# Kernel optimization log

Hardware: AMD Instinct MI355X
Metric: run time of the kernel (lower is better)

## Reference

```python
import jax, jax.numpy as jnp
import numpy as np

NEG_SLOPE = 0.2  # PyG GATConv default negative_slope


def _gat_layer(x, src, dst, W, a_src, a_dst, b, heads, ch, concat, num_nodes):
    # x: [Nt, Fin]; W: [Fin, heads*ch]; a_src/a_dst: [heads, ch]
    xw = (x @ W).reshape(num_nodes, heads, ch)            # [Nt, H, C]
    alpha_s = jnp.sum(xw * a_src, axis=-1)                # [Nt, H]
    alpha_d = jnp.sum(xw * a_dst, axis=-1)                # [Nt, H]
    e = jax.nn.leaky_relu(alpha_s[src] + alpha_d[dst], NEG_SLOPE)  # [E, H]
    # segment softmax over destination nodes (every node has a self-loop)
    m = jax.lax.stop_gradient(jax.ops.segment_max(e, dst, num_segments=num_nodes))
    ex = jnp.exp(e - m[dst])
    denom = jax.ops.segment_sum(ex, dst, num_segments=num_nodes)
    alpha = ex / (denom[dst] + 1e-16)                     # [E, H]
    out = jax.ops.segment_sum(alpha[:, :, None] * xw[src], dst, num_segments=num_nodes)  # [Nt, H, C]
    out = out.reshape(num_nodes, heads * ch) if concat else out.mean(axis=1)
    return out + b


def setup_inputs() -> dict:
    key = jax.random.key(0)
    ks = jax.random.split(key, 12)
    B, N, IN, HID, H, OUT, E = 2, 10000, 256, 256, 2, 256, 160000
    x = jax.random.normal(ks[0], (B, N, IN), dtype=jnp.float32)
    edge_index = jax.random.randint(ks[1], (2, E), 0, N, dtype=jnp.int32)
    s_in = 1.0 / np.sqrt(IN)
    s_h = 1.0 / np.sqrt(HID)
    s_hh = 1.0 / np.sqrt(HID * H)
    W1 = jax.random.normal(ks[2], (IN, H * HID), dtype=jnp.float32) * s_in
    att_src1 = jax.random.normal(ks[3], (H, HID), dtype=jnp.float32) * s_h
    att_dst1 = jax.random.normal(ks[4], (H, HID), dtype=jnp.float32) * s_h
    b1 = jax.random.normal(ks[5], (H * HID,), dtype=jnp.float32) * 0.01
    W2 = jax.random.normal(ks[6], (H * HID, OUT), dtype=jnp.float32) * s_hh
    att_src2 = jax.random.normal(ks[7], (1, OUT), dtype=jnp.float32) * s_h
    att_dst2 = jax.random.normal(ks[8], (1, OUT), dtype=jnp.float32) * s_h
    b2 = jax.random.normal(ks[9], (OUT,), dtype=jnp.float32) * 0.01
    return {"x": x, "edge_index": edge_index, "W1": W1, "att_src1": att_src1,
            "att_dst1": att_dst1, "b1": b1, "W2": W2, "att_src2": att_src2,
            "att_dst2": att_dst2, "b2": b2}


def reference(x, edge_index, W1, att_src1, att_dst1, b1, W2, att_src2, att_dst2, b2):
    B, N, C = x.shape
    H, HID = att_src1.shape
    OUT = W2.shape[1]
    Nt = B * N
    xf = x.reshape(Nt, C)
    # batch edge index with per-graph node offsets (shared edges across batch)
    offs = (jnp.arange(B, dtype=edge_index.dtype) * N)       # [B]
    ei = (edge_index[:, None, :] + offs[None, :, None]).reshape(2, -1)  # [2, B*E]
    # add self loops (PyG GATConv default)
    loops = jnp.arange(Nt, dtype=edge_index.dtype)
    src = jnp.concatenate([ei[0], loops])
    dst = jnp.concatenate([ei[1], loops])
    h = _gat_layer(xf, src, dst, W1, att_src1, att_dst1, b1, H, HID, True, Nt)
    h = jax.nn.gelu(h, approximate=False)  # torch F.gelu default = exact erf
    out = _gat_layer(h, src, dst, W2, att_src2, att_dst2, b2, 1, OUT, False, Nt)
    return out.reshape(B, N, OUT)
```

## Files before the change

### kernel.cpp

```cpp
#include <hip/hip_runtime.h>
#include <math.h>

constexpr int B_   = 2;
constexpr int N_   = 10000;
constexpr int IN_  = 256;
constexpr int HID_ = 256;
constexpr int H1_  = 2;
constexpr int OUT_ = 256;
constexpr int E_   = 160000;
constexpr int NT_  = B_ * N_;
constexpr float SLOPE = 0.2f;
constexpr int DMAX = 128;

typedef unsigned short u16;
typedef __attribute__((ext_vector_type(8))) short short8;
typedef __attribute__((ext_vector_type(4))) float f32x4;

__device__ __forceinline__ u16 f2bf(float f) {
    unsigned int u = __float_as_uint(f);
    u += 0x7fffu + ((u >> 16) & 1u);
    return (u16)(u >> 16);
}
__device__ __forceinline__ void bf8(uint4 r, float4& lo, float4& hi) {
    lo = make_float4(__uint_as_float((r.x & 0xffffu) << 16),
                     __uint_as_float(r.x & 0xffff0000u),
                     __uint_as_float((r.y & 0xffffu) << 16),
                     __uint_as_float(r.y & 0xffff0000u));
    hi = make_float4(__uint_as_float((r.z & 0xffffu) << 16),
                     __uint_as_float(r.z & 0xffff0000u),
                     __uint_as_float((r.w & 0xffffu) << 16),
                     __uint_as_float(r.w & 0xffff0000u));
}
__device__ __forceinline__ void fma4(float4& a, float s, float4 v) {
    a.x = fmaf(s, v.x, a.x); a.y = fmaf(s, v.y, a.y);
    a.z = fmaf(s, v.z, a.z); a.w = fmaf(s, v.w, a.w);
}
__device__ __forceinline__ float lrelu(float e) { return (e < 0.f) ? SLOPE * e : e; }

__device__ __forceinline__ void g2l16(const void* g, void* l) {
    __builtin_amdgcn_global_load_lds(
        (const __attribute__((address_space(1))) unsigned int*)g,
        (__attribute__((address_space(3))) unsigned int*)l, 16, 0, 0);
}

__global__ __launch_bounds__(256) void k_wprep(
    const float* __restrict__ W1,
    const float* __restrict__ aS1, const float* __restrict__ aD1,
    const float* __restrict__ W2,
    const float* __restrict__ aS2, const float* __restrict__ aD2,
    float* __restrict__ w1s, float* __restrict__ w1d,
    float* __restrict__ w2s, float* __restrict__ w2d,
    u16* __restrict__ W1t, u16* __restrict__ W2t,
    uint4* __restrict__ zbase) {
    __shared__ float tld[32][33];
    const int blk = blockIdx.x;
    if (blk < 16) {
        for (int i = blk * 256 + threadIdx.x; i < 12500; i += 16 * 256)
            zbase[i] = make_uint4(0, 0, 0, 0);
    } else if (blk < 528) {
        int wv = (blk - 16) * 4 + (threadIdx.x >> 6);
        int lane = threadIdx.x & 63;
        int c = lane * 4;
        float4 wr, av;
        if (wv < 1024) {
            int h = (wv >> 8) & 1;
            int k = wv & 255;
            const float* a = (wv < 512) ? aS1 : aD1;
            wr = *(const float4*)(W1 + (size_t)k * 512 + h * 256 + c);
            av = *(const float4*)(a + h * 256 + c);
        } else {
            int k = (wv - 1024) & 511;
            const float* a = (wv < 1536) ? aS2 : aD2;
            wr = *(const float4*)(W2 + (size_t)k * 256 + c);
            av = *(const float4*)(a + c);
        }
        float s = wr.x * av.x + wr.y * av.y + wr.z * av.z + wr.w * av.w;
        #pragma unroll
        for (int off = 32; off; off >>= 1) s += __shfl_down(s, off);
        if (lane == 0) {
            if (wv < 512)       w1s[wv] = s;
            else if (wv < 1024) w1d[wv - 512] = s;
            else if (wv < 1536) w2s[wv - 1024] = s;
            else                w2d[wv - 1536] = s;
        }
    } else {
        const int b = blk - 528;
        const int z = b >> 7;
        const int bb = b & 127;
        const float* S = z ? W2 : W1;
        u16* D = z ? W2t : W1t;
        const int R = z ? 512 : 256;
        const int C = z ? 256 : 512;
        const int xt = C >> 5;
        const int bx = bb % xt, by = bb / xt;
        const int tx = threadIdx.x & 31, ty = threadIdx.x >> 5;
        int xx = bx * 32 + tx;
        int y0 = by * 32 + ty;
        #pragma unroll
        for (int i = 0; i < 32; i += 8)
            tld[ty + i][tx] = S[(size_t)(y0 + i) * C + xx];
        __syncthreads();
        int xo = by * 32 + tx;
        int yo = bx * 32 + ty;
        #pragma unroll
        for (int i = 0; i < 32; i += 8)
            D[(size_t)(yo + i) * R + xo] = f2bf(tld[tx][ty + i]);
    }
}

__global__ __launch_bounds__(256) void k_pre(
    const float* __restrict__ x, u16* __restrict__ Xb,
    const float* __restrict__ w1s, const float* __restrict__ w1d,
    float* __restrict__ as1, float* __restrict__ ad1,
    const int* __restrict__ ei, int* __restrict__ cnt, int* __restrict__ bucket) {
    const int NB = NT_ / 4;
    if ((int)blockIdx.x < NB) {
        const int w = threadIdx.x >> 6, lane = threadIdx.x & 63;
        const int nt = blockIdx.x * 4 + w;
        const int c = lane * 4;
        float4 v = *(const float4*)(x + (size_t)nt * 256 + c);
        ((uint2*)(Xb + (size_t)nt * 256))[lane] =
            make_uint2((unsigned)f2bf(v.x) | ((unsigned)f2bf(v.y) << 16),
                       (unsigned)f2bf(v.z) | ((unsigned)f2bf(v.w) << 16));
        float4 s0v = *(const float4*)(w1s + c);
        float4 s1v = *(const float4*)(w1s + 256 + c);
        float4 d0v = *(const float4*)(w1d + c);
        float4 d1v = *(const float4*)(w1d + 256 + c);
        float s0 = v.x*s0v.x + v.y*s0v.y + v.z*s0v.z + v.w*s0v.w;
        float s1 = v.x*s1v.x + v.y*s1v.y + v.z*s1v.z + v.w*s1v.w;
        float d0 = v.x*d0v.x + v.y*d0v.y + v.z*d0v.z + v.w*d0v.w;
        float d1 = v.x*d1v.x + v.y*d1v.y + v.z*d1v.z + v.w*d1v.w;
        #pragma unroll
        for (int off = 32; off; off >>= 1) {
            s0 += __shfl_down(s0, off); s1 += __shfl_down(s1, off);
            d0 += __shfl_down(d0, off); d1 += __shfl_down(d1, off);
        }
        if (lane == 0) {
            as1[nt * 2] = s0; as1[nt * 2 + 1] = s1;
            ad1[nt * 2] = d0; ad1[nt * 2 + 1] = d1;
        }
    } else {
        int e = (blockIdx.x - NB) * 256 + threadIdx.x;
        if (e < E_) {
            int s = ei[e], d = ei[E_ + e];
            int p = atomicAdd(&cnt[d], 1);
            if (p < DMAX - 1) bucket[d * DMAX + p] = s;
        }
    }
}

__global__ __launch_bounds__(256) void k_agg1x(
    const u16* __restrict__ Xb,
    const float* __restrict__ as_, const float* __restrict__ ad_,
    const int* __restrict__ cnt, const int* __restrict__ bucket,
    u16* __restrict__ Y) {
    __shared__ int   stl[4][DMAX];
    __shared__ float exw[4][2 * DMAX];
    const int w    = threadIdx.x >> 6;
    const int lane = threadIdx.x & 63;
    const int half = lane >> 5;
    const int l32  = lane & 31;
    const int nt   = blockIdx.x * 4 + w;
    if (nt >= NT_) return;
    const int nl   = nt % N_;
    const int boff = nt - nl;
    const int r0   = nl * DMAX;
    int deg = cnt[nl]; deg = (deg < DMAX - 1) ? deg : (DMAX - 1);
    const float adv0 = ad_[nt * 2], adv1 = ad_[nt * 2 + 1];
    const float adv = half ? adv1 : adv0;

    for (int i = lane; i <= deg; i += 64)
        stl[w][i] = (i < deg) ? (bucket[r0 + i] + boff) : nt;

    float den = 0.f;
    for (int i = l32; i <= deg; i += 32) {
        int st = stl[w][i];
        float ex = __expf(lrelu(as_[st * 2 + half] + adv));
        exw[w][2 * i + half] = ex;
        den += ex;
    }
    #pragma unroll
    for (int off = 16; off; off >>= 1) den += __shfl_xor(den, off);
    const float inv = 1.f / (den + 1e-16f);
    const float invO = __shfl_xor(inv, 32);

    const int slot = half;
    const int nin = deg + 1;
    const u16* fb = Xb + l32 * 8;
    float4 A0l = {0,0,0,0}, A0h = {0,0,0,0}, A1l = {0,0,0,0}, A1h = {0,0,0,0};
    float4 B0l = {0,0,0,0}, B0h = {0,0,0,0}, B1l = {0,0,0,0}, B1h = {0,0,0,0};
    int j = 0;
    for (; j + 8 <= nin; j += 8) {
        int sA = stl[w][j + slot],     sB = stl[w][j + 2 + slot];
        int sC = stl[w][j + 4 + slot], sD = stl[w][j + 6 + slot];
        float2 wA = *(const float2*)&exw[w][2 * (j + slot)];
        float2 wB = *(const float2*)&exw[w][2 * (j + 2 + slot)];
        float2 wC = *(const float2*)&exw[w][2 * (j + 4 + slot)];
        float2 wD = *(const float2*)&exw[w][2 * (j + 6 + slot)];
        uint4 vA = *(const uint4*)(fb + (size_t)sA * 256);
        uint4 vB = *(const uint4*)(fb + (size_t)sB * 256);
        uint4 vC = *(const uint4*)(fb + (size_t)sC * 256);
        uint4 vD = *(const uint4*)(fb + (size_t)sD * 256);
        float4 lo, hi;
        bf8(vA, lo, hi); fma4(A0l, wA.x, lo); fma4(A0h, wA.x, hi);
                         fma4(A1l, wA.y, lo); fma4(A1h, wA.y, hi);
        bf8(vB, lo, hi); fma4(B0l, wB.x, lo); fma4(B0h, wB.x, hi);
                         fma4(B1l, wB.y, lo); fma4(B1h, wB.y, hi);
        bf8(vC, lo, hi); fma4(A0l, wC.x, lo); fma4(A0h, wC.x, hi);
                         fma4(A1l, wC.y, lo); fma4(A1h, wC.y, hi);
        bf8(vD, lo, hi); fma4(B0l, wD.x, lo); fma4(B0h, wD.x, hi);
                         fma4(B1l, wD.y, lo); fma4(B1h, wD.y, hi);
    }
    for (int jj = j + slot; jj < nin; jj += 2) {
        int s0 = stl[w][jj];
        float2 w01 = *(const float2*)&exw[w][2 * jj];
        uint4 v0 = *(const uint4*)(fb + (size_t)s0 * 256);
        float4 lo, hi;
        bf8(v0, lo, hi); fma4(A0l, w01.x, lo); fma4(A0h, w01.x, hi);
                         fma4(A1l, w01.y, lo); fma4(A1h, w01.y, hi);
    }
    A0l.x += B0l.x; A0l.y += B0l.y; A0l.z += B0l.z; A0l.w += B0l.w;
    A0h.x += B0h.x; A0h.y += B0h.y; A0h.z += B0h.z; A0h.w += B0h.w;
    A1l.x += B1l.x; A1l.y += B1l.y; A1l.z += B1l.z; A1l.w += B1l.w;
    A1h.x += B1h.x; A1h.y += B1h.y; A1h.z += B1h.z; A1h.w += B1h.w;
    A0l.x += __shfl_xor(A0l.x, 32); A0l.y += __shfl_xor(A0l.y, 32);
    A0l.z += __shfl_xor(A0l.z, 32); A0l.w += __shfl_xor(A0l.w, 32);
    A0h.x += __shfl_xor(A0h.x, 32); A0h.y += __shfl_xor(A0h.y, 32);
    A0h.z += __shfl_xor(A0h.z, 32); A0h.w += __shfl_xor(A0h.w, 32);
    A1l.x += __shfl_xor(A1l.x, 32); A1l.y += __shfl_xor(A1l.y, 32);
    A1l.z += __shfl_xor(A1l.z, 32); A1l.w += __shfl_xor(A1l.w, 32);
    A1h.x += __shfl_xor(A1h.x, 32); A1h.y += __shfl_xor(A1h.y, 32);
    A1h.z += __shfl_xor(A1h.z, 32); A1h.w += __shfl_xor(A1h.w, 32);

    if (slot == 0) {
        float f0[8] = { A0l.x*inv,  A0l.y*inv,  A0l.z*inv,  A0l.w*inv,
                        A0h.x*inv,  A0h.y*inv,  A0h.z*inv,  A0h.w*inv };
        float f1[8] = { A1l.x*invO, A1l.y*invO, A1l.z*invO, A1l.w*invO,
                        A1h.x*invO, A1h.y*invO, A1h.z*invO, A1h.w*invO };
        size_t ob = (size_t)nt * 512 + l32 * 8;
        *(uint4*)(Y + ob) =
            make_uint4((unsigned)f2bf(f0[0]) | ((unsigned)f2bf(f0[1]) << 16),
                       (unsigned)f2bf(f0[2]) | ((unsigned)f2bf(f0[3]) << 16),
                       (unsigned)f2bf(f0[4]) | ((unsigned)f2bf(f0[5]) << 16),
                       (unsigned)f2bf(f0[6]) | ((unsigned)f2bf(f0[7]) << 16));
        *(uint4*)(Y + ob + 256) =
            make_uint4((unsigned)f2bf(f1[0]) | ((unsigned)f2bf(f1[1]) << 16),
                       (unsigned)f2bf(f1[2]) | ((unsigned)f2bf(f1[3]) << 16),
                       (unsigned)f2bf(f1[4]) | ((unsigned)f2bf(f1[5]) << 16),
                       (unsigned)f2bf(f1[6]) | ((unsigned)f2bf(f1[7]) << 16));
    }
}

__global__ __launch_bounds__(256, 5) void gemm_g(
    const u16* __restrict__ Yf, const u16* __restrict__ W1t,
    u16* __restrict__ Hb,
    const float* __restrict__ b1,
    const float* __restrict__ w2s, const float* __restrict__ w2d,
    float* __restrict__ as2, float* __restrict__ ad2, int M) {
    __shared__ u16 sA[2][64 * 64], sB[2][64 * 64];
    const int tid = threadIdx.x, wave = tid >> 6, lane = tid & 63;
    const int bm = blockIdx.x, bn = blockIdx.y, h = blockIdx.z;

    const int rsel = lane >> 3;
    const int kc   = ((lane & 7) ^ rsel) * 8;
    int rA0 = bm * 64 + wave * 16 + rsel;
    int rA1 = rA0 + 8;
    rA0 = (rA0 < M) ? rA0 : (M - 1);
    rA1 = (rA1 < M) ? rA1 : (M - 1);
    const int rB = bn * 64 + wave * 16 + rsel;
    const u16* gA0 = Yf + (size_t)rA0 * 512 + h * 256 + kc;
    const u16* gA1 = Yf + (size_t)rA1 * 512 + h * 256 + kc;
    const u16* gB0 = W1t + (size_t)(h * 256 + rB) * 256 + kc;
    const u16* gB1 = W1t + (size_t)(h * 256 + rB + 8) * 256 + kc;
    const int lofs = wave * 1024;

    const int wm = wave & 1, wn = wave >> 1;
    const int l15 = lane & 15, quad = lane >> 4;
    const int sw  = l15 & 7;
    const int aR0 = (wm * 32 + l15) * 64; const int aR1 = aR0 + 1024;
    const int bR0 = (wn * 32 + l15) * 64; const int bR1 = bR0 + 1024;
    const int c0 = (quad ^ sw) * 8;
    const int c1 = ((4 + quad) ^ sw) * 8;

    f32x4 acc[2][2];
    #pragma unroll
    for (int i = 0; i < 2; i++)
        #pragma unroll
        for (int j = 0; j < 2; j++)
            acc[i][j] = (f32x4){0.f, 0.f, 0.f, 0.f};

    auto stage = [&](int k0, int b) {
        g2l16(gA0 + k0, &sA[b][lofs]);       g2l16(gA1 + k0, &sA[b][lofs + 512]);
        g2l16(gB0 + k0, &sB[b][lofs]);       g2l16(gB1 + k0, &sB[b][lofs + 512]);
    };
    auto compute = [&](const u16* A_, const u16* B_) {
        short8 a0 = *(const short8*)(A_ + aR0 + c0);
        short8 a1 = *(const short8*)(A_ + aR1 + c0);
        short8 b0 = *(const short8*)(B_ + bR0 + c0);
        short8 b1v = *(const short8*)(B_ + bR1 + c0);
        acc[0][0] = __builtin_amdgcn_mfma_f32_16x16x32_bf16(a0, b0, acc[0][0], 0, 0, 0);
        acc[0][1] = __builtin_amdgcn_mfma_f32_16x16x32_bf16(a0, b1v, acc[0][1], 0, 0, 0);
        acc[1][0] = __builtin_amdgcn_mfma_f32_16x16x32_bf16(a1, b0, acc[1][0], 0, 0, 0);
        acc[1][1] = __builtin_amdgcn_mfma_f32_16x16x32_bf16(a1, b1v, acc[1][1], 0, 0, 0);
        a0 = *(const short8*)(A_ + aR0 + c1);
        a1 = *(const short8*)(A_ + aR1 + c1);
        b0 = *(const short8*)(B_ + bR0 + c1);
        b1v = *(const short8*)(B_ + bR1 + c1);
        acc[0][0] = __builtin_amdgcn_mfma_f32_16x16x32_bf16(a0, b0, acc[0][0], 0, 0, 0);
        acc[0][1] = __builtin_amdgcn_mfma_f32_16x16x32_bf16(a0, b1v, acc[0][1], 0, 0, 0);
        acc[1][0] = __builtin_amdgcn_mfma_f32_16x16x32_bf16(a1, b0, acc[1][0], 0, 0, 0);
        acc[1][1] = __builtin_amdgcn_mfma_f32_16x16x32_bf16(a1, b1v, acc[1][1], 0, 0, 0);
    };

    stage(0, 0);
    __syncthreads();
    stage(64, 1);  compute(sA[0], sB[0]); __syncthreads();
    stage(128, 0); compute(sA[1], sB[1]); __syncthreads();
    stage(192, 1); compute(sA[0], sB[0]); __syncthreads();
                   compute(sA[1], sB[1]);

    const int colL = bn * 64 + wn * 32;
    float Bv[2], Sv[2], Dv[2];
    #pragma unroll
    for (int j = 0; j < 2; j++) {
        int cg = h * 256 + colL + j * 16 + l15;
        Bv[j] = b1[cg]; Sv[j] = w2s[cg]; Dv[j] = w2d[cg];
    }
    #pragma unroll
    for (int i = 0; i < 2; i++) {
        #pragma unroll
        for (int r = 0; r < 4; r++) {
            int row = bm * 64 + wm * 32 + i * 16 + quad * 4 + r;
            float o[2], ps = 0.f, pd = 0.f;
            #pragma unroll
            for (int j = 0; j < 2; j++) {
                float v = acc[i][j][r] + Bv[j];
                v = 0.5f * v * (1.f + erff(v * 0.70710678118654752f));
                o[j] = v;
                ps = fmaf(v, Sv[j], ps);
                pd = fmaf(v, Dv[j], pd);
            }
            #pragma unroll
            for (int off = 1; off < 16; off <<= 1) {
                ps += __shfl_xor(ps, off);
                pd += __shfl_xor(pd, off);
            }
            if (row < M) {
                if (l15 == 0) { atomicAdd(&as2[row], ps); atomicAdd(&ad2[row], pd); }
                #pragma unroll
                for (int j = 0; j < 2; j++)
                    Hb[(size_t)row * 512 + h * 256 + colL + j * 16 + l15] = f2bf(o[j]);
            }
        }
    }
}

__global__ __launch_bounds__(256, 5) void gemm_p(
    const u16* __restrict__ A, const u16* __restrict__ Bt,
    u16* __restrict__ C16, int M, int N, int K) {
    __shared__ u16 sA[2][64 * 64], sB[2][64 * 64];
    const int tid = threadIdx.x, wave = tid >> 6, lane = tid & 63;
    const int bm = blockIdx.x, bn = blockIdx.y;

    const int rsel = lane >> 3;
    const int kc   = ((lane & 7) ^ rsel) * 8;
    int rA0 = bm * 64 + wave * 16 + rsel;
    int rA1 = rA0 + 8;
    rA0 = (rA0 < M) ? rA0 : (M - 1);
    rA1 = (rA1 < M) ? rA1 : (M - 1);
    const int rB = bn * 64 + wave * 16 + rsel;
    const u16* gA0 = A + (size_t)rA0 * K + kc;
    const u16* gA1 = A + (size_t)rA1 * K + kc;
    const u16* gB0 = Bt + (size_t)rB * K + kc;
    const u16* gB1 = Bt + (size_t)(rB + 8) * K + kc;
    const int lofs = wave * 1024;

    const int wm = wave & 1, wn = wave >> 1;
    const int l15 = lane & 15, quad = lane >> 4;
    const int sw  = l15 & 7;
    const int aR0 = (wm * 32 + l15) * 64; const int aR1 = aR0 + 1024;
    const int bR0 = (wn * 32 + l15) * 64; const int bR1 = bR0 + 1024;
    const int c0 = (quad ^ sw) * 8;
    const int c1 = ((4 + quad) ^ sw) * 8;

    f32x4 acc[2][2];
    #pragma unroll
    for (int i = 0; i < 2; i++)
        #pragma unroll
        for (int j = 0; j < 2; j++)
            acc[i][j] = (f32x4){0.f, 0.f, 0.f, 0.f};

    auto stage = [&](int k0, int b) {
        g2l16(gA0 + k0, &sA[b][lofs]);       g2l16(gA1 + k0, &sA[b][lofs + 512]);
        g2l16(gB0 + k0, &sB[b][lofs]);       g2l16(gB1 + k0, &sB[b][lofs + 512]);
    };
    auto compute = [&](const u16* A_, const u16* B_) {
        short8 a0 = *(const short8*)(A_ + aR0 + c0);
        short8 a1 = *(const short8*)(A_ + aR1 + c0);
        short8 b0 = *(const short8*)(B_ + bR0 + c0);
        short8 b1v = *(const short8*)(B_ + bR1 + c0);
        acc[0][0] = __builtin_amdgcn_mfma_f32_16x16x32_bf16(a0, b0, acc[0][0], 0, 0, 0);
        acc[0][1] = __builtin_amdgcn_mfma_f32_16x16x32_bf16(a0, b1v, acc[0][1], 0, 0, 0);
        acc[1][0] = __builtin_amdgcn_mfma_f32_16x16x32_bf16(a1, b0, acc[1][0], 0, 0, 0);
        acc[1][1] = __builtin_amdgcn_mfma_f32_16x16x32_bf16(a1, b1v, acc[1][1], 0, 0, 0);
        a0 = *(const short8*)(A_ + aR0 + c1);
        a1 = *(const short8*)(A_ + aR1 + c1);
        b0 = *(const short8*)(B_ + bR0 + c1);
        b1v = *(const short8*)(B_ + bR1 + c1);
        acc[0][0] = __builtin_amdgcn_mfma_f32_16x16x32_bf16(a0, b0, acc[0][0], 0, 0, 0);
        acc[0][1] = __builtin_amdgcn_mfma_f32_16x16x32_bf16(a0, b1v, acc[0][1], 0, 0, 0);
        acc[1][0] = __builtin_amdgcn_mfma_f32_16x16x32_bf16(a1, b0, acc[1][0], 0, 0, 0);
        acc[1][1] = __builtin_amdgcn_mfma_f32_16x16x32_bf16(a1, b1v, acc[1][1], 0, 0, 0);
    };

    const int nt = K >> 6;
    stage(0, 0);
    __syncthreads();
    for (int t = 0; t < nt; t += 2) {
        if (t + 1 < nt) stage((t + 1) << 6, 1);
        compute(sA[0], sB[0]);
        __syncthreads();
        if (t + 2 < nt) stage((t + 2) << 6, 0);
        compute(sA[1], sB[1]);
        __syncthreads();
    }

    #pragma unroll
    for (int i = 0; i < 2; i++) {
        #pragma unroll
        for (int r = 0; r < 4; r++) {
            int row = bm * 64 + wm * 32 + i * 16 + quad * 4 + r;
            if (row < M) {
                #pragma unroll
                for (int j = 0; j < 2; j++) {
                    int col = bn * 64 + wn * 32 + j * 16 + l15;
                    C16[(size_t)row * N + col] = f2bf(acc[i][j][r]);
                }
            }
        }
    }
}

__global__ __launch_bounds__(256) void k_agg_h1(
    const u16* __restrict__ feat,
    const float* __restrict__ as_, const float* __restrict__ ad_,
    const int* __restrict__ cnt, const int* __restrict__ bucket,
    const float* __restrict__ bias,
    float* __restrict__ out) {
    __shared__ int   stl[4][DMAX];
    __shared__ float exw[4][DMAX];
    const int w    = threadIdx.x >> 6;
    const int lane = threadIdx.x & 63;
    const int slot = lane >> 5;
    const int l32  = lane & 31;
    const int nt   = blockIdx.x * 4 + w;
    if (nt >= NT_) return;
    const int nl   = nt % N_;
    const int boff = nt - nl;
    const int r0   = nl * DMAX;
    int deg = cnt[nl]; deg = (deg < DMAX - 1) ? deg : (DMAX - 1);
    const float adv = ad_[nt];

    for (int i = lane; i <= deg; i += 64)
        stl[w][i] = (i < deg) ? (bucket[r0 + i] + boff) : nt;

    float den = 0.f;
    for (int i = lane; i <= deg; i += 64) {
        int st = stl[w][i];
        float ex = __expf(lrelu(as_[st] + adv));
        exw[w][i] = ex;
        den += ex;
    }
    #pragma unroll
    for (int off = 32; off; off >>= 1) den += __shfl_xor(den, off);
    const float inv = 1.f / (den + 1e-16f);

    const int nin = deg + 1;
    const u16* fb = feat + l32 * 8;
    float4 aA0 = {0,0,0,0}, aB0 = {0,0,0,0}, aA1 = {0,0,0,0}, aB1 = {0,0,0,0};
    int j = 0;
    for (; j + 8 <= nin; j += 8) {
        int sA = stl[w][j + slot],     sB = stl[w][j + 2 + slot];
        int sC = stl[w][j + 4 + slot], sD = stl[w][j + 6 + slot];
        float wA = exw[w][j + slot],     wB = exw[w][j + 2 + slot];
        float wC = exw[w][j + 4 + slot], wD = exw[w][j + 6 + slot];
        uint4 vA = *(const uint4*)(fb + (size_t)sA * 256);
        uint4 vB = *(const uint4*)(fb + (size_t)sB * 256);
        uint4 vC = *(const uint4*)(fb + (size_t)sC * 256);
        uint4 vD = *(const uint4*)(fb + (size_t)sD * 256);
        float4 lo, hi;
        bf8(vA, lo, hi); fma4(aA0, wA, lo); fma4(aB0, wA, hi);
        bf8(vB, lo, hi); fma4(aA1, wB, lo); fma4(aB1, wB, hi);
        bf8(vC, lo, hi); fma4(aA0, wC, lo); fma4(aB0, wC, hi);
        bf8(vD, lo, hi); fma4(aA1, wD, lo); fma4(aB1, wD, hi);
    }
    for (; j + 4 <= nin; j += 4) {
        int sA = stl[w][j + slot], sB = stl[w][j + 2 + slot];
        float wA = exw[w][j + slot], wB = exw[w][j + 2 + slot];
        uint4 vA = *(const uint4*)(fb + (size_t)sA * 256);
        uint4 vB = *(const uint4*)(fb + (size_t)sB * 256);
        float4 lo, hi;
        bf8(vA, lo, hi); fma4(aA0, wA, lo); fma4(aB0, wA, hi);
        bf8(vB, lo, hi); fma4(aA1, wB, lo); fma4(aB1, wB, hi);
    }
    for (int jj = j + slot; jj < nin; jj += 2) {
        int s0 = stl[w][jj];
        float w0 = exw[w][jj];
        uint4 v0 = *(const uint4*)(fb + (size_t)s0 * 256);
        float4 lo, hi;
        bf8(v0, lo, hi); fma4(aA0, w0, lo); fma4(aB0, w0, hi);
    }
    aA0.x += aA1.x; aA0.y += aA1.y; aA0.z += aA1.z; aA0.w += aA1.w;
    aB0.x += aB1.x; aB0.y += aB1.y; aB0.z += aB1.z; aB0.w += aB1.w;
    aA0.x += __shfl_xor(aA0.x, 32); aA0.y += __shfl_xor(aA0.y, 32);
    aA0.z += __shfl_xor(aA0.z, 32); aA0.w += __shfl_xor(aA0.w, 32);
    aB0.x += __shfl_xor(aB0.x, 32); aB0.y += __shfl_xor(aB0.y, 32);
    aB0.z += __shfl_xor(aB0.z, 32); aB0.w += __shfl_xor(aB0.w, 32);

    if (slot == 0) {
        int c = l32 * 8;
        float4 b0 = *(const float4*)(bias + c);
        float4 b1 = *(const float4*)(bias + c + 4);
        float* ob = out + (size_t)nt * 256 + c;
        *(float4*)(ob)     = make_float4(aA0.x * inv + b0.x, aA0.y * inv + b0.y,
                                         aA0.z * inv + b0.z, aA0.w * inv + b0.w);
        *(float4*)(ob + 4) = make_float4(aB0.x * inv + b1.x, aB0.y * inv + b1.y,
                                         aB0.z * inv + b1.z, aB0.w * inv + b1.w);
    }
}

extern "C" void kernel_launch(void* const* d_in, const int* in_sizes, int n_in,
                              void* d_out, int out_size, void* d_ws, size_t ws_size,
                              hipStream_t stream) {
    const float* x    = (const float*)d_in[0];
    const int*   ei   = (const int*)  d_in[1];
    const float* W1   = (const float*)d_in[2];
    const float* aS1  = (const float*)d_in[3];
    const float* aD1  = (const float*)d_in[4];
    const float* b1   = (const float*)d_in[5];
    const float* W2   = (const float*)d_in[6];
    const float* aS2  = (const float*)d_in[7];
    const float* aD2  = (const float*)d_in[8];
    const float* b2   = (const float*)d_in[9];
    float* out = (float*)d_out;

    u16* Xb   = (u16*)d_ws;
    u16* Y    = Xb + (size_t)NT_ * 256;
    u16* Hb   = Y  + (size_t)NT_ * 512;
    u16* hw16 = Hb + (size_t)NT_ * 512;
    float* as1 = (float*)(hw16 + (size_t)NT_ * 256);
    float* ad1 = as1 + NT_ * H1_;
    float* as2 = ad1 + NT_ * H1_;
    float* ad2 = as2 + NT_;
    int* cnt   = (int*)(ad2 + NT_);
    int* bucket= cnt + N_;
    u16* W1t   = (u16*)(bucket + N_ * DMAX);
    u16* W2t   = W1t + 512 * 256;
    float* w1s = (float*)(W2t + 256 * 512);
    float* w1d = w1s + 512;
    float* w2s = w1d + 512;
    float* w2d = w2s + 512;

    k_wprep<<<784, 256, 0, stream>>>(W1, aS1, aD1, W2, aS2, aD2,
                                     w1s, w1d, w2s, w2d, W1t, W2t, (uint4*)as2);

    k_pre<<<NT_ / 4 + (E_ + 255) / 256, 256, 0, stream>>>(
        x, Xb, w1s, w1d, as1, ad1, ei, cnt, bucket);

    k_agg1x<<<(NT_ + 3) / 4, 256, 0, stream>>>(Xb, as1, ad1, cnt, bucket, Y);
    gemm_g<<<dim3((NT_ + 63) / 64, 4, 2), 256, 0, stream>>>(
        Y, W1t, Hb, b1, w2s, w2d, as2, ad2, NT_);

    gemm_p<<<dim3((NT_ + 63) / 64, OUT_ / 64), 256, 0, stream>>>(
        Hb, W2t, hw16, NT_, OUT_, H1_ * HID_);
    k_agg_h1<<<(NT_ + 3) / 4, 256, 0, stream>>>(hw16, as2, ad2, cnt, bucket, b2, out);
}
```

Measured before the change: 193.2 us.

## Retile layer-2 projection GEMM to 64x128 tiles with single-buffered K=32 steps

Rewrites gemm_p to compute 64x128 output tiles (each wave 32x64, eight MFMAs per K-step) instead of 64x64, halving the grid's N dimension so each A tile is read once per 128 output columns. It also drops the double-buffered 64-wide K staging with XOR swizzle in favour of a simple single-buffer 32-wide K loop with two barriers per step, and removes the occupancy hint in launch bounds. The aim is more reuse of A and more MFMAs per LDS load. The cost is losing load/compute overlap and the bank-conflict swizzle, plus twice as many barriers per unit of K.

```diff
diff --git a/kernel.cpp b/kernel.cpp
--- a/kernel.cpp
+++ b/kernel.cpp
@@ -355,76 +355,52 @@
     }
 }
 
-__global__ __launch_bounds__(256, 5) void gemm_p(
+__global__ __launch_bounds__(256) void gemm_p(
     const u16* __restrict__ A, const u16* __restrict__ Bt,
     u16* __restrict__ C16, int M, int N, int K) {
-    __shared__ u16 sA[2][64 * 64], sB[2][64 * 64];
+    __shared__ u16 sA[64 * 32], sB[128 * 32];
     const int tid = threadIdx.x, wave = tid >> 6, lane = tid & 63;
     const int bm = blockIdx.x, bn = blockIdx.y;
-
-    const int rsel = lane >> 3;
-    const int kc   = ((lane & 7) ^ rsel) * 8;
-    int rA0 = bm * 64 + wave * 16 + rsel;
-    int rA1 = rA0 + 8;
-    rA0 = (rA0 < M) ? rA0 : (M - 1);
-    rA1 = (rA1 < M) ? rA1 : (M - 1);
-    const int rB = bn * 64 + wave * 16 + rsel;
-    const u16* gA0 = A + (size_t)rA0 * K + kc;
-    const u16* gA1 = A + (size_t)rA1 * K + kc;
-    const u16* gB0 = Bt + (size_t)rB * K + kc;
-    const u16* gB1 = Bt + (size_t)(rB + 8) * K + kc;
-    const int lofs = wave * 1024;
+    const int srow = 16 * wave + (lane >> 2);
+    const int kc   = (lane & 3) * 8;
+    int rA = bm * 64 + srow;  rA = (rA < M) ? rA : (M - 1);
+    const int rB0 = bn * 128 + srow; const int rB1 = rB0 + 64;
+    const u16* gA  = A  + (size_t)rA  * K + kc;
+    const u16* gB0 = Bt + (size_t)rB0 * K + kc;
+    const u16* gB1 = Bt + (size_t)rB1 * K + kc;
+    u16* lA  = sA + wave * 512;
+    u16* lB0 = sB + wave * 512;  u16* lB1 = lB0 + 2048;
 
     const int wm = wave & 1, wn = wave >> 1;
     const int l15 = lane & 15, quad = lane >> 4;
-    const int sw  = l15 & 7;
-    const int aR0 = (wm * 32 + l15) * 64; const int aR1 = aR0 + 1024;
-    const int bR0 = (wn * 32 + l15) * 64; const int bR1 = bR0 + 1024;
-    const int c0 = (quad ^ sw) * 8;
-    const int c1 = ((4 + quad) ^ sw) * 8;
-
-    f32x4 acc[2][2];
+    const int aOff = (wm * 32 + l15) * 32 + quad * 8;
+    const int bOff = (wn * 64 + l15) * 32 + quad * 8;
+
+    f32x4 acc[2][4];
     #pragma unroll
     for (int i = 0; i < 2; i++)
         #pragma unroll
-        for (int j = 0; j < 2; j++)
+        for (int j = 0; j < 4; j++)
             acc[i][j] = (f32x4){0.f, 0.f, 0.f, 0.f};
 
-    auto stage = [&](int k0, int b) {
-        g2l16(gA0 + k0, &sA[b][lofs]);       g2l16(gA1 + k0, &sA[b][lofs + 512]);
-        g2l16(gB0 + k0, &sB[b][lofs]);       g2l16(gB1 + k0, &sB[b][lofs + 512]);
-    };
-    auto compute = [&](const u16* A_, const u16* B_) {
-        short8 a0 = *(const short8*)(A_ + aR0 + c0);
-        short8 a1 = *(const short8*)(A_ + aR1 + c0);
-        short8 b0 = *(const short8*)(B_ + bR0 + c0);
-        short8 b1v = *(const short8*)(B_ + bR1 + c0);
-        acc[0][0] = __builtin_amdgcn_mfma_f32_16x16x32_bf16(a0, b0, acc[0][0], 0, 0, 0);
-        acc[0][1] = __builtin_amdgcn_mfma_f32_16x16x32_bf16(a0, b1v, acc[0][1], 0, 0, 0);
-        acc[1][0] = __builtin_amdgcn_mfma_f32_16x16x32_bf16(a1, b0, acc[1][0], 0, 0, 0);
-        acc[1][1] = __builtin_amdgcn_mfma_f32_16x16x32_bf16(a1, b1v, acc[1][1], 0, 0, 0);
-        a0 = *(const short8*)(A_ + aR0 + c1);
-        a1 = *(const short8*)(A_ + aR1 + c1);
-        b0 = *(const short8*)(B_ + bR0 + c1);
-        b1v = *(const short8*)(B_ + bR1 + c1);
-        acc[0][0] = __builtin_amdgcn_mfma_f32_16x16x32_bf16(a0, b0, acc[0][0], 0, 0, 0);
-        acc[0][1] = __builtin_amdgcn_mfma_f32_16x16x32_bf16(a0, b1v, acc[0][1], 0, 0, 0);
-        acc[1][0] = __builtin_amdgcn_mfma_f32_16x16x32_bf16(a1, b0, acc[1][0], 0, 0, 0);
-        acc[1][1] = __builtin_amdgcn_mfma_f32_16x16x32_bf16(a1, b1v, acc[1][1], 0, 0, 0);
-    };
-
-    const int nt = K >> 6;
-    stage(0, 0);
-    __syncthreads();
-    for (int t = 0; t < nt; t += 2) {
-        if (t + 1 < nt) stage((t + 1) << 6, 1);
-        compute(sA[0], sB[0]);
+    for (int k0 = 0; k0 < K; k0 += 32) {
+        g2l16(gA + k0, lA);
+        g2l16(gB0 + k0, lB0); g2l16(gB1 + k0, lB1);
         __syncthreads();
-        if (t + 2 < nt) stage((t + 2) << 6, 0);
-        compute(sA[1], sB[1]);
+        short8 af[2], bf[4];
+        #pragma unroll
+        for (int i = 0; i < 2; i++)
+            af[i] = *(const short8*)(sA + aOff + i * 512);
+        #pragma unroll
+        for (int j = 0; j < 4; j++)
+            bf[j] = *(const short8*)(sB + bOff + j * 512);
+        #pragma unroll
+        for (int i = 0; i < 2; i++)
+            #pragma unroll
+            for (int j = 0; j < 4; j++)
+                acc[i][j] = __builtin_amdgcn_mfma_f32_16x16x32_bf16(af[i], bf[j], acc[i][j], 0, 0, 0);
         __syncthreads();
     }
-
     #pragma unroll
     for (int i = 0; i < 2; i++) {
         #pragma unroll
@@ -432,8 +408,8 @@
             int row = bm * 64 + wm * 32 + i * 16 + quad * 4 + r;
             if (row < M) {
                 #pragma unroll
-                for (int j = 0; j < 2; j++) {
-                    int col = bn * 64 + wn * 32 + j * 16 + l15;
+                for (int j = 0; j < 4; j++) {
+                    int col = bn * 128 + wn * 64 + j * 16 + l15;
                     C16[(size_t)row * N + col] = f2bf(acc[i][j][r]);
                 }
             }
@@ -571,7 +547,7 @@
     gemm_g<<<dim3((NT_ + 63) / 64, 4, 2), 256, 0, stream>>>(
         Y, W1t, Hb, b1, w2s, w2d, as2, ad2, NT_);
 
-    gemm_p<<<dim3((NT_ + 63) / 64, OUT_ / 64), 256, 0, stream>>>(
+    gemm_p<<<dim3((NT_ + 63) / 64, OUT_ / 128), 256, 0, stream>>>(
         Hb, W2t, hw16, NT_, OUT_, H1_ * HID_);
     k_agg_h1<<<(NT_ + 3) / 4, 256, 0, stream>>>(hw16, as2, ad2, cnt, bucket, b2, out);
 }
```

New measurement: 188.9 us. 2.2% less time.
